# Kernel tuning notes

Measured on AMD Instinct MI355X. Metric: run time of the kernel, lower is better.

Reference implementation:

```python
import jax, jax.numpy as jnp
import numpy as np

WS = 14            # window height/width
CLS = 1            # cls tokens
DIM = 768
H = 12             # heads
DH = DIM // H      # head dim = 64
B = 128
N = WS * WS + CLS  # 197
SCALE = DH ** (-0.5)
TABLE = (2 * WS - 1) ** 2 + CLS  # 730


def _rel_index():
    # Swin-style relative position index, with CLS rows/cols pointing at the
    # last table entry (torch uses index -1 which wraps to TABLE-1).
    c = np.arange(WS)
    coords = np.stack(np.meshgrid(c, c, indexing='ij'))      # [2,14,14]
    cf = coords.reshape(2, -1)                                # [2,196]
    rel = cf[:, :, None] - cf[:, None, :]                     # [2,196,196]
    rel = rel.transpose(1, 2, 0).astype(np.int64)             # [196,196,2]
    rel[..., 0] += WS - 1
    rel[..., 1] += WS - 1
    rel[..., 0] *= 2 * WS - 1
    idx = rel.sum(-1)                                         # [196,196]
    full = np.full((N, N), -1, np.int64)
    full[CLS:, CLS:] = idx
    full = np.where(full < 0, TABLE - 1, full)
    return jnp.asarray(full, jnp.int32)


def setup_inputs() -> dict:
    key = jax.random.key(0)
    ks = jax.random.split(key, 5)
    return {
        'x': jax.random.normal(ks[0], (B, N, DIM), jnp.float32),
        'qkv_w': jax.random.normal(ks[1], (3 * DIM, DIM), jnp.float32) * 0.02,
        'proj_w': jax.random.normal(ks[2], (DIM, DIM), jnp.float32) * 0.02,
        'proj_b': jnp.zeros((DIM,), jnp.float32),
        'bias_table': jax.random.normal(ks[3], (TABLE, H), jnp.float32) * 0.02,
        'rel_idx': _rel_index(),
    }


def reference(x, qkv_w, proj_w, proj_b, bias_table, rel_idx):
    Bc, Nc, C = x.shape
    qkv = x @ qkv_w.T                                   # [B,N,3C]
    qkv = qkv.reshape(Bc, Nc, 3, H, DH).transpose(2, 0, 3, 1, 4)
    q, k, v = qkv[0], qkv[1], qkv[2]                    # [B,H,N,D]
    attn = jnp.einsum('bhnd,bhmd->bhnm', q, k) * SCALE  # [B,H,N,N]
    bias = bias_table[rel_idx]                          # [N,N,H]
    attn = attn + bias.transpose(2, 0, 1)[None]         # broadcast over batch
    attn = jax.nn.softmax(attn, axis=-1)
    out = jnp.einsum('bhnm,bhmd->bhnd', attn, v)        # [B,H,N,D]
    out = out.transpose(0, 2, 1, 3).reshape(Bc, Nc, C)
    return out @ proj_w.T + proj_b
```

## Files before the change

kernel.cpp:

```cpp
#include <hip/hip_runtime.h>
#include <hip/hip_bf16.h>

typedef _Float16 half8 __attribute__((ext_vector_type(8)));
typedef _Float16 half4 __attribute__((ext_vector_type(4)));
typedef float floatx4 __attribute__((ext_vector_type(4)));

#define MFMA16(a, b, c) __builtin_amdgcn_mfma_f32_16x16x32_f16(a, b, c, 0, 0, 0)
#define GLDS16(gp, lp) __builtin_amdgcn_global_load_lds( \
    (const __attribute__((address_space(1))) void*)(gp), \
    (__attribute__((address_space(3))) void*)(lp), 16, 0, 0)

#define BATCH 128
#define NTOK 197
#define NPAD 208
#define DIM 768
#define NH 12
#define DH 64
#define M_ROWS (BATCH * NTOK)
#define MP_ROWS (BATCH * NPAD)
#define KPAD 224
#define NKT 13
#define NTILES (BATCH * NH * NKT)

#define PREP_X (MP_ROWS * (DIM / 8))
#define PREP_WQ (3 * DIM * DIM / 8)
#define PREP_WP (DIM * DIM / 8)
#define PREP_B (NH * 13 * 13 * 256)
#define PREP_TOT (PREP_X + PREP_WQ + PREP_WP + PREP_B)

#define BAR() __asm__ volatile("s_barrier" ::: "memory")
#define VMW4() __asm__ volatile("s_waitcnt vmcnt(4)" ::: "memory")
#define VMW0() __asm__ volatile("s_waitcnt vmcnt(0)" ::: "memory")

#define STG(gp, lp) do { \
    GLDS16((gp), (lp)); \
    GLDS16((gp) + 64 * DIM, (lp) + 4096); } while (0)

__device__ __forceinline__ half8 cvt8(const float* s) {
    float4 v0 = *(const float4*)s;
    float4 v1 = *(const float4*)(s + 4);
    half8 o;
    o[0] = (_Float16)v0.x; o[1] = (_Float16)v0.y;
    o[2] = (_Float16)v0.z; o[3] = (_Float16)v0.w;
    o[4] = (_Float16)v1.x; o[5] = (_Float16)v1.y;
    o[6] = (_Float16)v1.z; o[7] = (_Float16)v1.w;
    return o;
}

__global__ void prep_kernel(const float* __restrict__ x,
                            const float* __restrict__ qkv_w,
                            const float* __restrict__ proj_w,
                            const float* __restrict__ table,
                            const int* __restrict__ ridx,
                            _Float16* __restrict__ xh,
                            _Float16* __restrict__ wqkvh,
                            _Float16* __restrict__ wprojh,
                            _Float16* __restrict__ biasph) {
    int idx = blockIdx.x * 256 + threadIdx.x;
    if (idx < PREP_X) {
        int row = idx / (DIM / 8), ch = idx - row * (DIM / 8);
        int b = row / NPAD, n = row - b * NPAD;
        half8 o = {};
        if (n < NTOK) o = cvt8(x + (size_t)(b * NTOK + n) * DIM + ch * 8);
        *(half8*)&xh[(size_t)row * DIM + ch * 8] = o;
        return;
    }
    idx -= PREP_X;
    if (idx < PREP_WQ) {
        *(half8*)&wqkvh[idx * 8] = cvt8(qkv_w + idx * 8);
        return;
    }
    idx -= PREP_WQ;
    if (idx < PREP_WP) {
        *(half8*)&wprojh[idx * 8] = cvt8(proj_w + idx * 8);
        return;
    }
    idx -= PREP_WP;
    if (idx < PREP_B) {
        int e = idx & 255;
        int r = e >> 4, q = (e >> 2) & 3, rr = e & 3;
        int t = idx >> 8;
        int nt = t % 13; int t2 = t / 13; int qt = t2 % 13; int h = t2 / 13;
        int row = qt * 16 + q * 4 + rr;
        int col = nt * 16 + r;
        float v = -30000.0f;
        if (col < NTOK) {
            int rc = row < NTOK ? row : NTOK - 1;
            v = table[ridx[rc * NTOK + col] * NH + h];
        }
        biasph[idx] = (_Float16)v;
    }
}

template <int VM, bool STA, bool STB>
__device__ __forceinline__ void qkv_tile(int t, _Float16* smem,
                                         const _Float16* ga0, const _Float16* ga1,
                                         const _Float16* gb0, const _Float16* gb1,
                                         int sbase, int r, int q, int wm, int wn,
                                         floatx4 (&acc)[8][4]) {
    const int buf = t & 1;
    const int r7 = r & 7;
    const int sl0 = (q ^ r7) * 8;
    const int sl1 = sl0 ^ 32;
    _Float16* base = smem + buf * 32768;
    const _Float16* Ab = base + wm * 8192 + r * 64;
    const _Float16* Bb = base + 16384 + (wn >> 1) * 8192 + ((wn & 1) * 64 + r) * 64;
    _Float16* sA0 = smem + (buf ^ 1) * 32768 + sbase;
    _Float16* sA1 = sA0 + 8192;
    _Float16* sB0 = base + 16384 + sbase;
    _Float16* sB1 = sB0 + 8192;
    const int kof1 = (t + 1) * 64, kof2 = (t + 2) * 64;

    half8 a[4][2], b[4][2];

#pragma unroll
    for (int i = 0; i < 4; ++i) {
        a[i][0] = *(const half8*)(Ab + i * 1024 + sl0);
        a[i][1] = *(const half8*)(Ab + i * 1024 + sl1);
    }
#pragma unroll
    for (int j = 0; j < 2; ++j) {
        b[j][0] = *(const half8*)(Bb + j * 1024 + sl0);
        b[j][1] = *(const half8*)(Bb + j * 1024 + sl1);
    }
    if (STA) STG(ga0 + kof1, sA0);
    BAR();
    __builtin_amdgcn_s_setprio(1);
#pragma unroll
    for (int s = 0; s < 2; ++s)
#pragma unroll
        for (int i = 0; i < 4; ++i)
#pragma unroll
            for (int j = 0; j < 2; ++j)
                acc[i][j] = MFMA16(a[i][s], b[j][s], acc[i][j]);
    __builtin_amdgcn_s_setprio(0);
    BAR();

#pragma unroll
    for (int j = 0; j < 2; ++j) {
        b[2 + j][0] = *(const half8*)(Bb + (2 + j) * 1024 + sl0);
        b[2 + j][1] = *(const half8*)(Bb + (2 + j) * 1024 + sl1);
    }
    if (STA) STG(ga1 + kof1, sA1);
    BAR();
    __builtin_amdgcn_s_setprio(1);
#pragma unroll
    for (int s = 0; s < 2; ++s)
#pragma unroll
        for (int i = 0; i < 4; ++i)
#pragma unroll
            for (int j = 0; j < 2; ++j)
                acc[i][2 + j] = MFMA16(a[i][s], b[2 + j][s], acc[i][2 + j]);
    __builtin_amdgcn_s_setprio(0);
    BAR();

#pragma unroll
    for (int i = 0; i < 4; ++i) {
        a[i][0] = *(const half8*)(Ab + (4 + i) * 1024 + sl0);
        a[i][1] = *(const half8*)(Ab + (4 + i) * 1024 + sl1);
    }
    if (STB) STG(gb0 + kof2, sB0);
    BAR();
    __builtin_amdgcn_s_setprio(1);
#pragma unroll
    for (int s = 0; s < 2; ++s)
#pragma unroll
        for (int i = 0; i < 4; ++i)
#pragma unroll
            for (int j = 0; j < 2; ++j)
                acc[4 + i][j] = MFMA16(a[i][s], b[j][s], acc[4 + i][j]);
    __builtin_amdgcn_s_setprio(0);
    BAR();

    if (STB) STG(gb1 + kof2, sB1);
    BAR();
    __builtin_amdgcn_s_setprio(1);
#pragma unroll
    for (int s = 0; s < 2; ++s)
#pragma unroll
        for (int i = 0; i < 4; ++i)
#pragma unroll
            for (int j = 0; j < 2; ++j)
                acc[4 + i][2 + j] = MFMA16(a[i][s], b[2 + j][s], acc[4 + i][2 + j]);
    __builtin_amdgcn_s_setprio(0);
    if (VM == 4) { VMW4(); }
    else if (VM == 0) { VMW0(); }
    BAR();
}

__global__ __launch_bounds__(512, 2) void qkv_gemm8(const _Float16* __restrict__ X,
                                                    const _Float16* __restrict__ W,
                                                    _Float16* __restrict__ qh,
                                                    _Float16* __restrict__ kh,
                                                    _Float16* __restrict__ vt) {
    __shared__ __align__(16) _Float16 smem[65536];
    const int tid = threadIdx.x;
    const int lane = tid & 63, wid = tid >> 6;
    const int r = lane & 15, q = lane >> 4;
    const int wm = wid >> 2, wn = wid & 3;

    const int id = blockIdx.x;
    const int swz = (id & 7) * 117 + (id >> 3);
    const int by = swz / 9, bx = swz - by * 9;
    const int m0b = by * 256, n0b = bx * 256;

    const int srow = wid * 8 + (lane >> 3);
    const int sch = (lane & 7) ^ (lane >> 3);
    const _Float16* ga0 = X + (size_t)(m0b + srow) * DIM + sch * 8;
    const _Float16* ga1 = ga0 + (size_t)128 * DIM;
    const _Float16* gb0 = W + (size_t)(n0b + srow) * DIM + sch * 8;
    const _Float16* gb1 = gb0 + (size_t)128 * DIM;
    const int sbase = wid * 512;

    floatx4 acc[8][4] = {};

    STG(ga0, smem + sbase);
    STG(ga1, smem + 8192 + sbase);
    STG(gb0, smem + 16384 + sbase);
    STG(gb1, smem + 24576 + sbase);
    STG(gb0 + 64, smem + 32768 + 16384 + sbase);
    STG(gb1 + 64, smem + 32768 + 24576 + sbase);
    VMW4();
    BAR();

#pragma unroll 2
    for (int t = 0; t < 10; ++t)
        qkv_tile<4, true, true>(t, smem, ga0, ga1, gb0, gb1, sbase, r, q, wm, wn, acc);
    qkv_tile<0, true, false>(10, smem, ga0, ga1, gb0, gb1, sbase, r, q, wm, wn, acc);
    qkv_tile<2, false, false>(11, smem, ga0, ga1, gb0, gb1, sbase, r, q, wm, wn, acc);

    __syncthreads();
    const int which = bx / 3;
    const int cb = (bx - which * 3) * 256;
    if (which == 2) {
#pragma unroll
        for (int hp = 0; hp < 2; ++hp) {
            if (wm == hp) {
#pragma unroll
                for (int i = 0; i < 8; ++i)
#pragma unroll
                    for (int j = 0; j < 4; ++j) {
                        half4 hv;
#pragma unroll
                        for (int rr = 0; rr < 4; ++rr) hv[rr] = (_Float16)acc[i][j][rr];
                        *(half4*)&smem[(wn * 64 + j * 16 + r) * 136 + i * 16 + q * 4] = hv;
                    }
            }
            __syncthreads();
#pragma unroll
            for (int p = 0; p < 8; ++p) {
                int idx = p * 512 + tid;
                int c = idx >> 4, g0 = (idx & 15) * 8;
                int grow = m0b + hp * 128 + g0;
                int b_idx = grow / NPAD, n_idx = grow - b_idx * NPAD;
                int vcol = cb + c;
                int hh = vcol >> 6, d = vcol & 63;
                half8 hv = *(const half8*)&smem[c * 136 + g0];
                *(half8*)&vt[((size_t)(b_idx * NH + hh) * DH + d) * KPAD + n_idx] = hv;
            }
            __syncthreads();
        }
    } else {
        const float scale = (which == 0) ? 0.125f : 1.0f;
        _Float16* dst = (which == 0) ? qh : kh;
#pragma unroll
        for (int hp = 0; hp < 2; ++hp) {
            if (wm == hp) {
#pragma unroll
                for (int i = 0; i < 8; ++i)
#pragma unroll
                    for (int j = 0; j < 4; ++j)
#pragma unroll
                        for (int rr = 0; rr < 4; ++rr)
                            smem[(i * 16 + q * 4 + rr) * 272 + wn * 64 + j * 16 + r] =
                                (_Float16)(acc[i][j][rr] * scale);
            }
            __syncthreads();
#pragma unroll
            for (int p = 0; p < 8; ++p) {
                int idx = p * 512 + tid;
                int g = idx >> 5, c0 = (idx & 31) * 8;
                int grow = m0b + hp * 128 + g;
                int b_idx = grow / NPAD, n_idx = grow - b_idx * NPAD;
                int colm = cb + c0;
                int hh = colm >> 6, d0 = colm & 63;
                half8 hv = *(const half8*)&smem[g * 272 + c0];
                *(half8*)&dst[((size_t)(b_idx * NH + hh) * NPAD + n_idx) * DH + d0] = hv;
            }
            __syncthreads();
        }
    }
}

__device__ __forceinline__ void gemm_core_768(const _Float16* __restrict__ A,
                                              const _Float16* __restrict__ B,
                                              int m0b, int n0b,
                                              _Float16* As, _Float16* Bs,
                                              floatx4 acc[4][4]) {
    const int lane = threadIdx.x & 63;
    const int w = threadIdx.x >> 6;
    const int r = lane & 15, q = lane >> 4;
    const int mo = (w & 1) * 64;
    const int no = (w >> 1) * 64;
    const int srow = w * 32 + (lane >> 3);
    const int gatom = (lane & 7) ^ (lane >> 3);
    const int rx = r & 7;

    const _Float16* pa[4];
    const _Float16* pb[4];
#pragma unroll
    for (int c = 0; c < 4; ++c) {
        pa[c] = A + (size_t)(m0b + srow + c * 8) * DIM + gatom * 8;
        pb[c] = B + (size_t)(n0b + srow + c * 8) * DIM + gatom * 8;
    }
    _Float16* ldsA = As + w * 2048;
    _Float16* ldsB = Bs + w * 2048;

    for (int kk = 0; kk < DIM / 64; ++kk) {
#pragma unroll
        for (int c = 0; c < 4; ++c) {
            GLDS16(pa[c], ldsA + c * 512);
            GLDS16(pb[c], ldsB + c * 512);
            pa[c] += 64;
            pb[c] += 64;
        }
        __syncthreads();
#pragma unroll
        for (int s = 0; s < 2; ++s) {
            half8 a[4], b[4];
#pragma unroll
            for (int i = 0; i < 4; ++i)
                a[i] = *(const half8*)&As[((mo + i * 16 + r) * 8 + ((s * 4 + q) ^ rx)) * 8];
#pragma unroll
            for (int j = 0; j < 4; ++j)
                b[j] = *(const half8*)&Bs[((no + j * 16 + r) * 8 + ((s * 4 + q) ^ rx)) * 8];
#pragma unroll
            for (int i = 0; i < 4; ++i)
#pragma unroll
                for (int j = 0; j < 4; ++j)
                    acc[i][j] = MFMA16(a[i], b[j], acc[i][j]);
        }
        __syncthreads();
    }
}

__global__ __launch_bounds__(256) void proj_gemm(const _Float16* __restrict__ A,
                                                 const _Float16* __restrict__ W,
                                                 const float* __restrict__ bias,
                                                 float* __restrict__ out) {
    __shared__ __align__(16) _Float16 As[128 * 64];
    __shared__ __align__(16) _Float16 Bs[128 * 64];
    const int lane = threadIdx.x & 63;
    const int w = threadIdx.x >> 6;
    const int r = lane & 15, q = lane >> 4;

    const int id = blockIdx.x;
    const int xcd = id & 7;
    const int lid = id >> 3;
    const int bx = lid % 6;
    const int by = xcd * 25 + lid / 6;
    if (by >= 197) return;
    const int m0b = by * 128;
    const int n0b = bx * 128;

    floatx4 acc[4][4] = {};
    gemm_core_768(A, W, m0b, n0b, As, Bs, acc);

    const int m0 = m0b + (w & 1) * 64;
    const int n0 = n0b + (w >> 1) * 64;
#pragma unroll
    for (int i = 0; i < 4; ++i) {
#pragma unroll
        for (int rr = 0; rr < 4; ++rr) {
            size_t grow = m0 + i * 16 + q * 4 + rr;
#pragma unroll
            for (int j = 0; j < 4; ++j) {
                int gcol = n0 + j * 16 + r;
                out[grow * DIM + gcol] = acc[i][j][rr] + bias[gcol];
            }
        }
    }
}

__global__ __launch_bounds__(256) void attn_kernel(const _Float16* __restrict__ qh,
                                                   const _Float16* __restrict__ kh,
                                                   const _Float16* __restrict__ vt,
                                                   const _Float16* __restrict__ biasph,
                                                   _Float16* __restrict__ ah) {
    __shared__ __align__(16) _Float16 P[4][16][40];
    const int w = threadIdx.x >> 6, lane = threadIdx.x & 63;
    const int r = lane & 15, q = lane >> 4;
    const int id0 = blockIdx.x;
    const int bid = (id0 & 7) * 624 + (id0 >> 3);
    const int T = bid * 4 + w;
    const int bh = T / 13;
    const int qt = T - bh * 13;
    const int b = bh / NH, h = bh - b * NH;
    const _Float16* Qb = qh + (size_t)bh * NPAD * DH;
    const _Float16* Kb = kh + (size_t)bh * NPAD * DH;
    const _Float16* Vtb = vt + (size_t)bh * DH * KPAD;

    half4 bf[NKT];
    const _Float16* bbase = biasph + (((size_t)h * 13 + qt) * 13) * 256 + r * 16 + q * 4;
#pragma unroll
    for (int nt = 0; nt < NKT; ++nt)
        bf[nt] = *(const half4*)(bbase + nt * 256);

    const int rowq = qt * 16 + r;
    half8 aq0 = *(const half8*)(Qb + (size_t)rowq * DH + q * 8);
    half8 aq1 = *(const half8*)(Qb + (size_t)rowq * DH + 32 + q * 8);

    floatx4 sacc[NKT] = {};
#pragma unroll
    for (int nt = 0; nt < NKT; ++nt) {
        int rowk = nt * 16 + r;
        half8 b0 = *(const half8*)(Kb + (size_t)rowk * DH + q * 8);
        half8 b1 = *(const half8*)(Kb + (size_t)rowk * DH + 32 + q * 8);
        sacc[nt] = MFMA16(aq0, b0, sacc[nt]);
        sacc[nt] = MFMA16(aq1, b1, sacc[nt]);
    }

    _Float16 pv[NKT][4];
#pragma unroll
    for (int rr = 0; rr < 4; ++rr) {
        float sv[NKT];
        float sm = 0.f;
#pragma unroll
        for (int nt = 0; nt < NKT; ++nt) {
            float e = __expf(sacc[nt][rr] + (float)bf[nt][rr]);
            sv[nt] = e;
            sm += e;
        }
#pragma unroll
        for (int m = 1; m <= 8; m <<= 1) sm += __shfl_xor(sm, m, 64);
        float inv = 1.0f / sm;
#pragma unroll
        for (int nt = 0; nt < NKT; ++nt)
            pv[nt][rr] = (_Float16)(sv[nt] * inv);
    }

    floatx4 oacc[4] = {};
    _Float16* Pw = &P[w][0][0];
#pragma unroll
    for (int kt = 0; kt < 7; ++kt) {
        const int nt0 = kt * 2, nt1 = kt * 2 + 1;
#pragma unroll
        for (int rr = 0; rr < 4; ++rr) {
            Pw[(q * 4 + rr) * 40 + r] = pv[nt0][rr];
            Pw[(q * 4 + rr) * 40 + 16 + r] = (nt1 < NKT) ? pv[nt1][rr] : (_Float16)0.0f;
        }
        __asm__ volatile("" ::: "memory");
        half8 ap = *(const half8*)&Pw[r * 40 + q * 8];
        __asm__ volatile("" ::: "memory");
#pragma unroll
        for (int dt = 0; dt < 4; ++dt) {
            half8 bv = *(const half8*)(Vtb + (size_t)(dt * 16 + r) * KPAD + kt * 32 + q * 8);
            oacc[dt] = MFMA16(ap, bv, oacc[dt]);
        }
    }

#pragma unroll
    for (int rr = 0; rr < 4; ++rr) {
        int row = qt * 16 + q * 4 + rr;
        if (row < NTOK) {
            size_t o = ((size_t)b * NTOK + row) * DIM + h * DH;
#pragma unroll
            for (int dt = 0; dt < 4; ++dt)
                ah[o + dt * 16 + r] = (_Float16)oacc[dt][rr];
        }
    }
}

extern "C" void kernel_launch(void* const* d_in, const int* in_sizes, int n_in,
                              void* d_out, int out_size, void* d_ws, size_t ws_size,
                              hipStream_t stream) {
    const float* x = (const float*)d_in[0];
    const float* qkv_w = (const float*)d_in[1];
    const float* proj_w = (const float*)d_in[2];
    const float* proj_b = (const float*)d_in[3];
    const float* table = (const float*)d_in[4];
    const int* ridx = (const int*)d_in[5];
    float* out = (float*)d_out;

    char* ws = (char*)d_ws;
    const size_t SZ_XP = (size_t)MP_ROWS * DIM * 2;
    const size_t SZ_WQKV = (size_t)3 * DIM * DIM * 2;
    const size_t SZ_WPROJ = (size_t)DIM * DIM * 2;
    const size_t SZ_QK = (size_t)BATCH * NH * NPAD * DH * 2;
    const size_t SZ_VT = (size_t)BATCH * NH * DH * KPAD * 2;
    const size_t SZ_BIAS = (size_t)NH * 13 * 13 * 256 * 2;

    _Float16* xh = (_Float16*)(ws + 0);
    _Float16* ah = (_Float16*)(ws + 0);
    _Float16* wqkvh = (_Float16*)(ws + SZ_XP);
    _Float16* wprojh = (_Float16*)(ws + SZ_XP + SZ_WQKV);
    _Float16* qh = (_Float16*)(ws + SZ_XP + SZ_WQKV + SZ_WPROJ);
    _Float16* kh = (_Float16*)(ws + SZ_XP + SZ_WQKV + SZ_WPROJ + SZ_QK);
    _Float16* vt = (_Float16*)(ws + SZ_XP + SZ_WQKV + SZ_WPROJ + 2 * SZ_QK);
    _Float16* biasph = (_Float16*)(ws + SZ_XP + SZ_WQKV + SZ_WPROJ + 2 * SZ_QK + SZ_VT);
    (void)SZ_BIAS; (void)ws_size; (void)n_in; (void)in_sizes; (void)out_size;

    prep_kernel<<<(PREP_TOT + 255) / 256, 256, 0, stream>>>(
        x, qkv_w, proj_w, table, ridx, xh, wqkvh, wprojh, biasph);
    qkv_gemm8<<<936, 512, 0, stream>>>(xh, wqkvh, qh, kh, vt);
    attn_kernel<<<NTILES / 4, 256, 0, stream>>>(qh, kh, vt, biasph, ah);
    proj_gemm<<<1200, 256, 0, stream>>>(ah, wprojh, proj_b, out);
}
```

Before: 400.3 us.

## Restructure attention to one block per head with K/V staged in LDS

```diff
diff --git a/kernel.cpp b/kernel.cpp
--- a/kernel.cpp
+++ b/kernel.cpp
@@ -20,13 +20,13 @@
 #define MP_ROWS (BATCH * NPAD)
 #define KPAD 224
 #define NKT 13
-#define NTILES (BATCH * NH * NKT)
 
 #define PREP_X (MP_ROWS * (DIM / 8))
 #define PREP_WQ (3 * DIM * DIM / 8)
 #define PREP_WP (DIM * DIM / 8)
 #define PREP_B (NH * 13 * 13 * 256)
-#define PREP_TOT (PREP_X + PREP_WQ + PREP_WP + PREP_B)
+#define PREP_VZ (BATCH * NH * DH * 2)
+#define PREP_TOT (PREP_X + PREP_WQ + PREP_WP + PREP_B + PREP_VZ)
 
 #define BAR() __asm__ volatile("s_barrier" ::: "memory")
 #define VMW4() __asm__ volatile("s_waitcnt vmcnt(4)" ::: "memory")
@@ -55,7 +55,8 @@
                             _Float16* __restrict__ xh,
                             _Float16* __restrict__ wqkvh,
                             _Float16* __restrict__ wprojh,
-                            _Float16* __restrict__ biasph) {
+                            _Float16* __restrict__ biasph,
+                            _Float16* __restrict__ vt) {
     int idx = blockIdx.x * 256 + threadIdx.x;
     if (idx < PREP_X) {
         int row = idx / (DIM / 8), ch = idx - row * (DIM / 8);
@@ -89,6 +90,13 @@
             v = table[ridx[rc * NTOK + col] * NH + h];
         }
         biasph[idx] = (_Float16)v;
+        return;
+    }
+    idx -= PREP_B;
+    if (idx < PREP_VZ) {
+        int row = idx >> 1, c = idx & 1;
+        half8 z = {};
+        *(half8*)&vt[(size_t)row * KPAD + 208 + c * 8] = z;
     }
 }
 
@@ -382,91 +390,109 @@
     }
 }
 
-__global__ __launch_bounds__(256) void attn_kernel(const _Float16* __restrict__ qh,
-                                                   const _Float16* __restrict__ kh,
-                                                   const _Float16* __restrict__ vt,
-                                                   const _Float16* __restrict__ biasph,
-                                                   _Float16* __restrict__ ah) {
-    __shared__ __align__(16) _Float16 P[4][16][40];
-    const int w = threadIdx.x >> 6, lane = threadIdx.x & 63;
+__global__ __launch_bounds__(832, 7) void attn_kernel(const _Float16* __restrict__ qh,
+                                                      const _Float16* __restrict__ kh,
+                                                      const _Float16* __restrict__ vt,
+                                                      const _Float16* __restrict__ biasph,
+                                                      _Float16* __restrict__ ah) {
+    __shared__ __align__(16) _Float16 smem[38016];
+    _Float16* Ks = smem;
+    _Float16* Vs = smem + 13312;
+    _Float16* Pb = smem + 29696;
+    const int tid = threadIdx.x;
+    const int w = tid >> 6, lane = tid & 63;
     const int r = lane & 15, q = lane >> 4;
-    const int id0 = blockIdx.x;
-    const int bid = (id0 & 7) * 624 + (id0 >> 3);
-    const int T = bid * 4 + w;
-    const int bh = T / 13;
-    const int qt = T - bh * 13;
+    const int xr = r & 7;
+    const int bh = ((blockIdx.x & 7) * 192) + (blockIdx.x >> 3);
     const int b = bh / NH, h = bh - b * NH;
-    const _Float16* Qb = qh + (size_t)bh * NPAD * DH;
     const _Float16* Kb = kh + (size_t)bh * NPAD * DH;
     const _Float16* Vtb = vt + (size_t)bh * DH * KPAD;
 
-    half4 bf[NKT];
-    const _Float16* bbase = biasph + (((size_t)h * 13 + qt) * 13) * 256 + r * 16 + q * 4;
-#pragma unroll
-    for (int nt = 0; nt < NKT; ++nt)
-        bf[nt] = *(const half4*)(bbase + nt * 256);
-
-    const int rowq = qt * 16 + r;
+#pragma unroll
+    for (int rd = 0; rd < 2; ++rd) {
+        int i = rd * 832 + tid;
+        int g = i >> 3;
+        int cs = (i & 7) ^ (g & 7);
+        GLDS16(Kb + (size_t)g * DH + cs * 8, Ks + (rd * 832 + w * 64) * 8);
+    }
+#pragma unroll
+    for (int rd = 0; rd < 3; ++rd) {
+        int j = rd * 832 + tid;
+        if (j < 2048) {
+            int g = j >> 5;
+            int cs = (j & 31) ^ (g & 7);
+            if (cs >= 28) cs = 0;
+            GLDS16(Vtb + (size_t)g * KPAD + cs * 8, Vs + (rd * 832 + w * 64) * 8);
+        }
+    }
+    __syncthreads();
+
+    const int rowq = w * 16 + r;
+    const _Float16* Qb = qh + (size_t)bh * NPAD * DH;
     half8 aq0 = *(const half8*)(Qb + (size_t)rowq * DH + q * 8);
     half8 aq1 = *(const half8*)(Qb + (size_t)rowq * DH + 32 + q * 8);
 
-    floatx4 sacc[NKT] = {};
+    const _Float16* bbase = biasph + (((size_t)h * 13 + w) * 13) * 256 + r * 16 + q * 4;
+    half4 pvh[NKT + 1];
+    float osum[4] = {0.f, 0.f, 0.f, 0.f};
 #pragma unroll
     for (int nt = 0; nt < NKT; ++nt) {
-        int rowk = nt * 16 + r;
-        half8 b0 = *(const half8*)(Kb + (size_t)rowk * DH + q * 8);
-        half8 b1 = *(const half8*)(Kb + (size_t)rowk * DH + 32 + q * 8);
-        sacc[nt] = MFMA16(aq0, b0, sacc[nt]);
-        sacc[nt] = MFMA16(aq1, b1, sacc[nt]);
-    }
-
-    _Float16 pv[NKT][4];
+        half4 bv = *(const half4*)(bbase + nt * 256);
+        floatx4 acc;
+        acc[0] = (float)bv[0]; acc[1] = (float)bv[1];
+        acc[2] = (float)bv[2]; acc[3] = (float)bv[3];
+        const _Float16* kr = Ks + (nt * 16 + r) * 64;
+        half8 b0 = *(const half8*)(kr + (q ^ xr) * 8);
+        half8 b1 = *(const half8*)(kr + ((q ^ xr) ^ 4) * 8);
+        acc = MFMA16(aq0, b0, acc);
+        acc = MFMA16(aq1, b1, acc);
+        half4 e4;
+#pragma unroll
+        for (int rr = 0; rr < 4; ++rr) {
+            float e = __expf(acc[rr]);
+            osum[rr] += e;
+            e4[rr] = (_Float16)e;
+        }
+        pvh[nt] = e4;
+    }
+    {
+        half4 z = {};
+        pvh[NKT] = z;
+    }
 #pragma unroll
     for (int rr = 0; rr < 4; ++rr) {
-        float sv[NKT];
-        float sm = 0.f;
-#pragma unroll
-        for (int nt = 0; nt < NKT; ++nt) {
-            float e = __expf(sacc[nt][rr] + (float)bf[nt][rr]);
-            sv[nt] = e;
-            sm += e;
-        }
-#pragma unroll
-        for (int m = 1; m <= 8; m <<= 1) sm += __shfl_xor(sm, m, 64);
-        float inv = 1.0f / sm;
-#pragma unroll
-        for (int nt = 0; nt < NKT; ++nt)
-            pv[nt][rr] = (_Float16)(sv[nt] * inv);
+#pragma unroll
+        for (int m = 1; m <= 8; m <<= 1) osum[rr] += __shfl_xor(osum[rr], m, 64);
     }
 
     floatx4 oacc[4] = {};
-    _Float16* Pw = &P[w][0][0];
+    _Float16* Pw = Pb + w * 640;
 #pragma unroll
     for (int kt = 0; kt < 7; ++kt) {
-        const int nt0 = kt * 2, nt1 = kt * 2 + 1;
 #pragma unroll
         for (int rr = 0; rr < 4; ++rr) {
-            Pw[(q * 4 + rr) * 40 + r] = pv[nt0][rr];
-            Pw[(q * 4 + rr) * 40 + 16 + r] = (nt1 < NKT) ? pv[nt1][rr] : (_Float16)0.0f;
+            Pw[(q * 4 + rr) * 40 + r] = pvh[kt * 2][rr];
+            Pw[(q * 4 + rr) * 40 + 16 + r] = pvh[kt * 2 + 1][rr];
         }
         __asm__ volatile("" ::: "memory");
         half8 ap = *(const half8*)&Pw[r * 40 + q * 8];
         __asm__ volatile("" ::: "memory");
 #pragma unroll
         for (int dt = 0; dt < 4; ++dt) {
-            half8 bv = *(const half8*)(Vtb + (size_t)(dt * 16 + r) * KPAD + kt * 32 + q * 8);
+            half8 bv = *(const half8*)(Vs + (dt * 16 + r) * 256 + (((kt * 4 + q) ^ xr) * 8));
             oacc[dt] = MFMA16(ap, bv, oacc[dt]);
         }
     }
 
 #pragma unroll
     for (int rr = 0; rr < 4; ++rr) {
-        int row = qt * 16 + q * 4 + rr;
+        int row = w * 16 + q * 4 + rr;
         if (row < NTOK) {
+            float inv = 1.0f / osum[rr];
             size_t o = ((size_t)b * NTOK + row) * DIM + h * DH;
 #pragma unroll
             for (int dt = 0; dt < 4; ++dt)
-                ah[o + dt * 16 + r] = (_Float16)oacc[dt][rr];
+                ah[o + dt * 16 + r] = (_Float16)(oacc[dt][rr] * inv);
         }
     }
 }
@@ -501,8 +527,8 @@
     (void)SZ_BIAS; (void)ws_size; (void)n_in; (void)in_sizes; (void)out_size;
 
     prep_kernel<<<(PREP_TOT + 255) / 256, 256, 0, stream>>>(
-        x, qkv_w, proj_w, table, ridx, xh, wqkvh, wprojh, biasph);
+        x, qkv_w, proj_w, table, ridx, xh, wqkvh, wprojh, biasph, vt);
     qkv_gemm8<<<936, 512, 0, stream>>>(xh, wqkvh, qh, kh, vt);
-    attn_kernel<<<NTILES / 4, 256, 0, stream>>>(qh, kh, vt, biasph, ah);
+    attn_kernel<<<BATCH * NH, 832, 0, stream>>>(qh, kh, vt, biasph, ah);
     proj_gemm<<<1200, 256, 0, stream>>>(ah, wprojh, proj_b, out);
 }
```

Measured after the change: 392.3 us. 1.02x faster.
